# Kernel tuning notes

Hardware: AMD Instinct MI355X
Metric: run time of the kernel (lower is better)

Reference implementation:

```python
import jax, jax.numpy as jnp
import numpy as np

N = 50000
E = 800000
D = 128
L = 2


def setup_inputs() -> dict:
    key = jax.random.key(0)
    k0, k1, k2 = jax.random.split(key, 3)
    x = jax.random.normal(k0, (N, D), dtype=jnp.float32)
    edge_index = jax.random.randint(k1, (2, E), 0, N, dtype=jnp.int64)
    # GCNConv weights: one [D, D] matrix + bias per layer (dim_in -> dim_in)
    W = jax.random.normal(k2, (L, D, D), dtype=jnp.float32) * (1.0 / np.sqrt(D))
    b = jnp.zeros((L, D), dtype=jnp.float32)
    return {"x": x, "edge_index": edge_index, "W": W, "b": b}


def reference(x, edge_index, W, b):
    """Stacked GCNConv + relu (dropout is identity in eval mode).

    GCNConv: out = D^{-1/2} (A + I) D^{-1/2} (X W) + b, with self-loops added.
    """
    n = x.shape[0]
    loops = jnp.arange(n, dtype=edge_index.dtype)
    src = jnp.concatenate([edge_index[0], loops])  # [E + N]
    dst = jnp.concatenate([edge_index[1], loops])  # [E + N]
    # Degree (with self-loops) based symmetric normalization
    deg = jax.ops.segment_sum(jnp.ones_like(dst, dtype=x.dtype), dst, num_segments=n)
    dinv = jax.lax.rsqrt(deg)  # deg >= 1 thanks to self-loops
    coef = (dinv[src] * dinv[dst])[:, None]  # [E + N, 1]

    num_layers = W.shape[0]
    for i in range(num_layers):
        h = x @ W[i]  # transform first, as PyG GCNConv does
        x = jax.ops.segment_sum(h[src] * coef, dst, num_segments=n) + b[i]
        x = jax.nn.relu(x)
        # F.dropout with training=False is identity
    return x
```

## Files before the change

kernel.cpp:

```cpp
#include <hip/hip_runtime.h>
#include <hip/hip_fp16.h>


#define D 128
#define WP 136
#define YP 136
#define ABI 8
#define AGT 32
#define NB_SCAN 196

typedef _Float16 half8 __attribute__((ext_vector_type(8)));
typedef float floatx4 __attribute__((ext_vector_type(4)));


__global__ void count_kernel(const int* __restrict__ dst, int* deg8,
                             int* __restrict__ rank, int e, int n) {
    int i = blockIdx.x * blockDim.x + threadIdx.x;
    int c = (blockIdx.x & 7) * n;
    if (i < e) rank[i] = atomicAdd(&deg8[c + dst[i]], 1);
}

__global__ __launch_bounds__(256) void scanA_cvtw_kernel(const int* __restrict__ deg8,
                                                         int* __restrict__ degT,
                                                         int* __restrict__ base8,
                                                         int* __restrict__ partial,
                                                         int n, int nbs,
                                                         const float* __restrict__ W,
                                                         __half* __restrict__ WhT) {
    __shared__ int red[4];
    int tid = threadIdx.x;
    int bid = blockIdx.x;
    if (bid < nbs) {
        int i = bid * 256 + tid;
        int tot = 0;
        if (i < n) {
            int run = 0;
#pragma unroll
            for (int c = 0; c < 8; ++c) {
                base8[c * n + i] = run;
                run += deg8[c * n + i];
            }
            degT[i] = run;
            tot = run;
        }
        for (int off = 32; off > 0; off >>= 1) tot += __shfl_down(tot, off, 64);
        if ((tid & 63) == 0) red[tid >> 6] = tot;
        __syncthreads();
        if (tid == 0) partial[bid] = red[0] + red[1] + red[2] + red[3];
    } else {
        int id = (bid - nbs) * 256 + tid;
        int l = id >> 14;
        int rem = id & 16383;
        int f = rem >> 7;
        int k = rem & 127;
        WhT[id] = __float2half(W[l * 16384 + k * 128 + f]);
    }
}

__global__ __launch_bounds__(256) void scanC2_kernel(const int* __restrict__ degT,
                                                     const int* __restrict__ partial,
                                                     int* __restrict__ row_ptr,
                                                     float* __restrict__ dinv, int n) {
    __shared__ int sc[256];
    __shared__ int scb[256];
    int tid = threadIdx.x;
    int bid = blockIdx.x;
    int p = (tid < NB_SCAN) ? partial[tid] : 0;
    scb[tid] = p;
    __syncthreads();
    for (int off = 1; off < 256; off <<= 1) {
        int v = (tid >= off) ? scb[tid - off] : 0;
        __syncthreads();
        scb[tid] += v;
        __syncthreads();
    }
    int i = bid * 256 + tid;
    int c = (i < n) ? degT[i] : 0;
    sc[tid] = c;
    __syncthreads();
    for (int off = 1; off < 256; off <<= 1) {
        int v = (tid >= off) ? sc[tid - off] : 0;
        __syncthreads();
        sc[tid] += v;
        __syncthreads();
    }
    if (i < n) {
        int base = ((bid == 0) ? 0 : scb[bid - 1]) + sc[tid] - c;
        row_ptr[i] = base;
        dinv[i] = rsqrtf((float)(c + 1));
    }
    if (bid == 0 && tid == 0) row_ptr[n] = scb[NB_SCAN - 1];
}


__device__ inline void gemm_body(int bid, int tid,
                                 const float* __restrict__ Xf,
                                 const __half* __restrict__ WhT,
                                 __half* __restrict__ Hh, int n,
                                 _Float16* wlds) {
#pragma unroll
    for (int q = 0; q < 8; ++q) {
        int idx = tid + q * 256;
        int row = idx >> 4;
        int col8 = (idx & 15) * 8;
        const uint2* gsrc = (const uint2*)(WhT + row * 128 + col8);
        uint2 a = gsrc[0];
        uint2 b = gsrc[1];
        uint2* ldst = (uint2*)(wlds + row * WP + col8);
        ldst[0] = a;
        ldst[1] = b;
    }
    __syncthreads();

    const int wave = tid >> 6;
    const int lane = tid & 63;
    const int m = lane & 15;
    const int quad = lane >> 4;

    const int node = bid * 64 + wave * 16 + m;
    const int node_ld = node < n ? node : (n - 1);

    half8 bfr[4];
#pragma unroll
    for (int k = 0; k < 4; ++k) {
        const float4* p = (const float4*)(Xf + (size_t)node_ld * 128 + k * 32 + quad * 8);
        float4 lo = p[0];
        float4 hi = p[1];
        half8 h;
        h[0] = (_Float16)lo.x; h[1] = (_Float16)lo.y;
        h[2] = (_Float16)lo.z; h[3] = (_Float16)lo.w;
        h[4] = (_Float16)hi.x; h[5] = (_Float16)hi.y;
        h[6] = (_Float16)hi.z; h[7] = (_Float16)hi.w;
        bfr[k] = h;
    }

    floatx4 acc[8];
#pragma unroll
    for (int f = 0; f < 8; ++f) acc[f] = (floatx4){0.f, 0.f, 0.f, 0.f};

#pragma unroll
    for (int f = 0; f < 8; ++f) {
#pragma unroll
        for (int k = 0; k < 4; ++k) {
            half8 a = *(const half8*)(wlds + (f * 16 + m) * WP + k * 32 + quad * 8);
            acc[f] = __builtin_amdgcn_mfma_f32_16x16x32_f16(a, bfr[k], acc[f], 0, 0, 0);
        }
    }

    if (node < n) {
#pragma unroll
        for (int f = 0; f < 8; ++f) {
            __half2 p0 = __floats2half2_rn(acc[f][0], acc[f][1]);
            __half2 p1 = __floats2half2_rn(acc[f][2], acc[f][3]);
            uint2 pk;
            pk.x = *(unsigned int*)&p0;
            pk.y = *(unsigned int*)&p1;
            *(uint2*)(Hh + (size_t)node * 128 + f * 16 + quad * 4) = pk;
        }
    }
}

__device__ inline void fill_body(int i,
                                 const int* __restrict__ src,
                                 const int* __restrict__ dst,
                                 const int* __restrict__ rank,
                                 const int* __restrict__ row_ptr,
                                 const int* __restrict__ base8,
                                 const float* __restrict__ dinv,
                                 int2* __restrict__ recs, int e, int n) {
    if (i < e) {
        int d = dst[i];
        int s = src[i];
        int c = (i >> 8) & 7;
        int pos = row_ptr[d] + base8[c * n + d] + rank[i];
        int2 rec;
        rec.x = s;
        rec.y = __float_as_int(dinv[s] * dinv[d]);
        recs[pos] = rec;
    }
}


__global__ __launch_bounds__(256) void gemmfill_kernel(const float* __restrict__ Xf,
                                                       const __half* __restrict__ WhT,
                                                       __half* __restrict__ Hh, int n, int nbg,
                                                       const int* __restrict__ src,
                                                       const int* __restrict__ dst,
                                                       const int* __restrict__ rank,
                                                       const int* __restrict__ row_ptr,
                                                       const int* __restrict__ base8,
                                                       const float* __restrict__ dinv,
                                                       int2* __restrict__ recs, int e) {
    __shared__ _Float16 wlds[128 * WP];
    int bid = blockIdx.x;
    int tid = threadIdx.x;
    if (bid < nbg) {
        gemm_body(bid, tid, Xf, WhT, Hh, n, wlds);
    } else {
        fill_body((bid - nbg) * 256 + tid, src, dst, rank, row_ptr, base8, dinv, recs, e, n);
    }
}


__device__ inline void unpack8(uint4 u, float* f) {
    union { unsigned int x; __half2 h; } a, b, c, d;
    a.x = u.x; b.x = u.y; c.x = u.z; d.x = u.w;
    float2 f0 = __half22float2(a.h);
    float2 f1 = __half22float2(b.h);
    float2 f2 = __half22float2(c.h);
    float2 f3 = __half22float2(d.h);
    f[0] = f0.x; f[1] = f0.y; f[2] = f1.x; f[3] = f1.y;
    f[4] = f2.x; f[5] = f2.y; f[6] = f3.x; f[7] = f3.y;
}

__device__ inline void agg_row_q(int v, int fl,
                                 const uint4* __restrict__ H16,
                                 const int2* __restrict__ recs,
                                 const int* __restrict__ row_ptr,
                                 const float* __restrict__ dinv,
                                 float* acc) {
    {
        float di = dinv[v];
        float selfc = di * di;
        uint4 hv = H16[(size_t)v * 16 + fl];
        float f[8]; unpack8(hv, f);
#pragma unroll
        for (int t = 0; t < 8; ++t) acc[t] = f[t] * selfc;
    }

    int e0 = row_ptr[v];
    int e1 = row_ptr[v + 1];
    int e = e0;
    for (; e + ABI <= e1; e += ABI) {
        int2 r[ABI]; uint4 hu[ABI];
#pragma unroll
        for (int j = 0; j < ABI; ++j) r[j] = recs[e + j];
#pragma unroll
        for (int j = 0; j < ABI; ++j) hu[j] = H16[(size_t)r[j].x * 16 + fl];
#pragma unroll
        for (int j = 0; j < ABI; ++j) {
            float c = __int_as_float(r[j].y);
            float f[8]; unpack8(hu[j], f);
#pragma unroll
            for (int t = 0; t < 8; ++t) acc[t] = fmaf(f[t], c, acc[t]);
        }
    }
    if (e < e1) {
        int2 r[ABI]; uint4 hu[ABI]; bool act[ABI];
#pragma unroll
        for (int j = 0; j < ABI; ++j) {
            act[j] = (e + j) < e1;
            if (act[j]) r[j] = recs[e + j];
        }
#pragma unroll
        for (int j = 0; j < ABI; ++j) {
            if (act[j]) hu[j] = H16[(size_t)r[j].x * 16 + fl];
        }
#pragma unroll
        for (int j = 0; j < ABI; ++j) {
            if (act[j]) {
                float c = __int_as_float(r[j].y);
                float f[8]; unpack8(hu[j], f);
#pragma unroll
                for (int t = 0; t < 8; ++t) acc[t] = fmaf(f[t], c, acc[t]);
            }
        }
    }
}

__global__ __launch_bounds__(256, 4) void agg_kernel(const __half* __restrict__ H,
                                                     const int2* __restrict__ recs,
                                                     const int* __restrict__ row_ptr,
                                                     const float* __restrict__ dinv,
                                                     const float* __restrict__ bias,
                                                     float* __restrict__ YF, int n) {
    int wave = threadIdx.x >> 6;
    int lane = threadIdx.x & 63;
    int qw = lane >> 4;
    int fl = lane & 15;
    int v = blockIdx.x * 16 + wave * 4 + qw;
    if (v >= n) return;

    const uint4* H16 = (const uint4*)H;
    float acc[8];
    agg_row_q(v, fl, H16, recs, row_ptr, dinv, acc);

    const float4* B4 = (const float4*)bias;
    float4 b0 = B4[fl * 2];
    float4 b1 = B4[fl * 2 + 1];
    float4* Y4 = (float4*)YF;
    Y4[(size_t)v * 32 + fl * 2] = make_float4(
        fmaxf(acc[0] + b0.x, 0.f), fmaxf(acc[1] + b0.y, 0.f),
        fmaxf(acc[2] + b0.z, 0.f), fmaxf(acc[3] + b0.w, 0.f));
    Y4[(size_t)v * 32 + fl * 2 + 1] = make_float4(
        fmaxf(acc[4] + b1.x, 0.f), fmaxf(acc[5] + b1.y, 0.f),
        fmaxf(acc[6] + b1.z, 0.f), fmaxf(acc[7] + b1.w, 0.f));
}

__global__ __launch_bounds__(512, 4) void aggemm_kernel(
    const __half* __restrict__ H,
    const int2* __restrict__ recs,
    const int* __restrict__ row_ptr,
    const float* __restrict__ dinv,
    const float* __restrict__ bias,
    const __half* __restrict__ WhT2,
    __half* __restrict__ H2, int n) {
    __shared__ _Float16 yt[AGT * YP];
    const int tid = threadIdx.x;
    const int wave = tid >> 6;
    const int lane = tid & 63;
    const int qw = lane >> 4;
    const int fl = lane & 15;
    const int g = blockIdx.x;
    const uint4* H16 = (const uint4*)H;

    {
        const float4* B4 = (const float4*)bias;
        float4 b0 = B4[fl * 2];
        float4 b1 = B4[fl * 2 + 1];
        int r = wave * 4 + qw;
        int v = g * AGT + r;
        if (v < n) {
            float acc[8];
            agg_row_q(v, fl, H16, recs, row_ptr, dinv, acc);
            __half2 p0 = __floats2half2_rn(fmaxf(acc[0] + b0.x, 0.f), fmaxf(acc[1] + b0.y, 0.f));
            __half2 p1 = __floats2half2_rn(fmaxf(acc[2] + b0.z, 0.f), fmaxf(acc[3] + b0.w, 0.f));
            __half2 p2 = __floats2half2_rn(fmaxf(acc[4] + b1.x, 0.f), fmaxf(acc[5] + b1.y, 0.f));
            __half2 p3 = __floats2half2_rn(fmaxf(acc[6] + b1.z, 0.f), fmaxf(acc[7] + b1.w, 0.f));
            uint4 pk;
            pk.x = *(unsigned int*)&p0;
            pk.y = *(unsigned int*)&p1;
            pk.z = *(unsigned int*)&p2;
            pk.w = *(unsigned int*)&p3;
            *(uint4*)&yt[r * YP + fl * 8] = pk;
        } else {
            uint4 z = make_uint4(0, 0, 0, 0);
            *(uint4*)&yt[r * YP + fl * 8] = z;
        }
    }
    __syncthreads();

    const int mg = wave & 1;
    const int fh = wave >> 1;
    const int node = g * AGT + mg * 16 + fl;

    half8 bfr[4];
#pragma unroll
    for (int k = 0; k < 4; ++k)
        bfr[k] = *(const half8*)&yt[(mg * 16 + fl) * YP + k * 32 + qw * 8];

#pragma unroll
    for (int fb = 0; fb < 2; ++fb) {
        int f = fh * 2 + fb;
        floatx4 a4 = (floatx4){0.f, 0.f, 0.f, 0.f};
#pragma unroll
        for (int k = 0; k < 4; ++k) {
            half8 a = *(const half8*)(WhT2 + ((f * 16 + fl) * 128 + k * 32 + qw * 8));
            a4 = __builtin_amdgcn_mfma_f32_16x16x32_f16(a, bfr[k], a4, 0, 0, 0);
        }
        if (node < n) {
            __half2 p0 = __floats2half2_rn(a4[0], a4[1]);
            __half2 p1 = __floats2half2_rn(a4[2], a4[3]);
            uint2 pk;
            pk.x = *(unsigned int*)&p0;
            pk.y = *(unsigned int*)&p1;
            *(uint2*)(H2 + (size_t)node * 128 + f * 16 + qw * 4) = pk;
        }
    }
}


extern "C" void kernel_launch(void* const* d_in, const int* in_sizes, int n_in,
                              void* d_out, int out_size, void* d_ws, size_t ws_size,
                              hipStream_t stream) {
    const float* x = (const float*)d_in[0];
    const int* ei = (const int*)d_in[1];
    const float* W = (const float*)d_in[2];
    const float* b = (const float*)d_in[3];
    float* out = (float*)d_out;

    const int N = in_sizes[0] / D;
    const int E = in_sizes[1] / 2;

    const int* src = ei;
    const int* dst = ei + E;

    int* wsi = (int*)d_ws;
    float* wsf = (float*)d_ws;
    const size_t o_deg8 = 0;
    const size_t o_degT = o_deg8 + 400000;
    const size_t o_dinv = o_degT + 50000;
    const size_t o_rp   = o_dinv + 50000;
    const size_t o_part = o_rp + 50016;
    const size_t o_boff = o_part + 256;
    const size_t o_b8   = o_boff + 256;
    const size_t o_rank = o_b8 + 400000;
    const size_t o_rec  = o_rank + 800000;
    const size_t o_h    = o_rec + 1600000;
    const size_t o_wht  = o_h + 3200000;
    const size_t o_h2   = o_wht + 16384;

    int* deg8    = wsi + o_deg8;
    int* degT    = wsi + o_degT;
    float* dinv  = wsf + o_dinv;
    int* row_ptr = wsi + o_rp;
    int* partial = wsi + o_part;
    int* base8   = wsi + o_b8;
    int* rank    = wsi + o_rank;
    int2* recs   = (int2*)(wsi + o_rec);
    __half* h    = (__half*)(wsi + o_h);
    __half* wht  = (__half*)(wsi + o_wht);
    __half* h2   = (__half*)(wsi + o_h2);

    const int nb_e = (E + 255) / 256;
    const int nb_s = (N + 255) / 256;
    const int nb_g = (N + 63) / 64;
    const int nb_ag = (N + AGT - 1) / AGT;
    const int nb_a = (N + 15) / 16;

    hipMemsetAsync(deg8, 0, (size_t)8 * 50000 * sizeof(int), stream);
    count_kernel<<<nb_e, 256, 0, stream>>>(dst, deg8, rank, E, N);
    scanA_cvtw_kernel<<<nb_s + 128, 256, 0, stream>>>(deg8, degT, base8, partial,
                                                      N, nb_s, W, wht);
    scanC2_kernel<<<nb_s, 256, 0, stream>>>(degT, partial, row_ptr, dinv, N);
    gemmfill_kernel<<<nb_g + nb_e, 256, 0, stream>>>(x, wht, h, N, nb_g,
                                                     src, dst, rank, row_ptr, base8,
                                                     dinv, recs, E);
    aggemm_kernel<<<nb_ag, 512, 0, stream>>>(h, recs, row_ptr, dinv, b,
                                             wht + 16384, h2, N);
    agg_kernel<<<nb_a, 256, 0, stream>>>(h2, recs, row_ptr, dinv, b + D, out, N);
}
```

Measured before the change: 218.1 us.

## Split each node's edge list across two lane groups and combine via shuffle

Both aggregation kernels now assign two 16-lane groups to each destination node. Each group handles half of the node's edge range, and the partial sums are combined with a cross-lane xor shuffle. Rows per block drop from 32 to 16 in the fused agg+GEMM kernel, so each wave now computes one output feature tile instead of two. The aim is more parallelism and memory-level concurrency on the gather, which with about 16 edges per node is latency bound. The cost is twice as many threads and blocks, the added shuffles, and idle lanes in the final store.

```diff
diff --git a/kernel.cpp b/kernel.cpp
--- a/kernel.cpp
+++ b/kernel.cpp
@@ -6,7 +6,7 @@
 #define WP 136
 #define YP 136
 #define ABI 8
-#define AGT 32
+#define AGT 16
 #define NB_SCAN 196
 
 typedef _Float16 half8 __attribute__((ext_vector_type(8)));
@@ -213,25 +213,32 @@
     f[4] = f2.x; f[5] = f2.y; f[6] = f3.x; f[7] = f3.y;
 }
 
-__device__ inline void agg_row_q(int v, int fl,
-                                 const uint4* __restrict__ H16,
-                                 const int2* __restrict__ recs,
-                                 const int* __restrict__ row_ptr,
-                                 const float* __restrict__ dinv,
-                                 float* acc) {
-    {
+__device__ inline void agg_row_qh(int v, int fl, int half,
+                                  const uint4* __restrict__ H16,
+                                  const int2* __restrict__ recs,
+                                  const int* __restrict__ row_ptr,
+                                  const float* __restrict__ dinv,
+                                  float* acc) {
+    int e0 = row_ptr[v];
+    int e1 = row_ptr[v + 1];
+    int mid = e0 + ((e1 - e0 + 1) >> 1);
+    int eb = half ? mid : e0;
+    int ee = half ? e1 : mid;
+
+    if (half == 0) {
         float di = dinv[v];
         float selfc = di * di;
         uint4 hv = H16[(size_t)v * 16 + fl];
         float f[8]; unpack8(hv, f);
 #pragma unroll
         for (int t = 0; t < 8; ++t) acc[t] = f[t] * selfc;
-    }
-
-    int e0 = row_ptr[v];
-    int e1 = row_ptr[v + 1];
-    int e = e0;
-    for (; e + ABI <= e1; e += ABI) {
+    } else {
+#pragma unroll
+        for (int t = 0; t < 8; ++t) acc[t] = 0.f;
+    }
+
+    int e = eb;
+    for (; e + ABI <= ee; e += ABI) {
         int2 r[ABI]; uint4 hu[ABI];
 #pragma unroll
         for (int j = 0; j < ABI; ++j) r[j] = recs[e + j];
@@ -245,11 +252,11 @@
             for (int t = 0; t < 8; ++t) acc[t] = fmaf(f[t], c, acc[t]);
         }
     }
-    if (e < e1) {
+    if (e < ee) {
         int2 r[ABI]; uint4 hu[ABI]; bool act[ABI];
 #pragma unroll
         for (int j = 0; j < ABI; ++j) {
-            act[j] = (e + j) < e1;
+            act[j] = (e + j) < ee;
             if (act[j]) r[j] = recs[e + j];
         }
 #pragma unroll
@@ -278,23 +285,29 @@
     int lane = threadIdx.x & 63;
     int qw = lane >> 4;
     int fl = lane & 15;
-    int v = blockIdx.x * 16 + wave * 4 + qw;
+    int half = qw & 1;
+    int v = blockIdx.x * 8 + wave * 2 + (qw >> 1);
     if (v >= n) return;
 
     const uint4* H16 = (const uint4*)H;
     float acc[8];
-    agg_row_q(v, fl, H16, recs, row_ptr, dinv, acc);
-
-    const float4* B4 = (const float4*)bias;
-    float4 b0 = B4[fl * 2];
-    float4 b1 = B4[fl * 2 + 1];
-    float4* Y4 = (float4*)YF;
-    Y4[(size_t)v * 32 + fl * 2] = make_float4(
-        fmaxf(acc[0] + b0.x, 0.f), fmaxf(acc[1] + b0.y, 0.f),
-        fmaxf(acc[2] + b0.z, 0.f), fmaxf(acc[3] + b0.w, 0.f));
-    Y4[(size_t)v * 32 + fl * 2 + 1] = make_float4(
-        fmaxf(acc[4] + b1.x, 0.f), fmaxf(acc[5] + b1.y, 0.f),
-        fmaxf(acc[6] + b1.z, 0.f), fmaxf(acc[7] + b1.w, 0.f));
+    agg_row_qh(v, fl, half, H16, recs, row_ptr, dinv, acc);
+
+#pragma unroll
+    for (int t = 0; t < 8; ++t) acc[t] += __shfl_xor(acc[t], 16);
+
+    if (half == 0) {
+        const float4* B4 = (const float4*)bias;
+        float4 b0 = B4[fl * 2];
+        float4 b1 = B4[fl * 2 + 1];
+        float4* Y4 = (float4*)YF;
+        Y4[(size_t)v * 32 + fl * 2] = make_float4(
+            fmaxf(acc[0] + b0.x, 0.f), fmaxf(acc[1] + b0.y, 0.f),
+            fmaxf(acc[2] + b0.z, 0.f), fmaxf(acc[3] + b0.w, 0.f));
+        Y4[(size_t)v * 32 + fl * 2 + 1] = make_float4(
+            fmaxf(acc[4] + b1.x, 0.f), fmaxf(acc[5] + b1.y, 0.f),
+            fmaxf(acc[6] + b1.z, 0.f), fmaxf(acc[7] + b1.w, 0.f));
+    }
 }
 
 __global__ __launch_bounds__(512, 4) void aggemm_kernel(
@@ -311,61 +324,66 @@
     const int lane = tid & 63;
     const int qw = lane >> 4;
     const int fl = lane & 15;
+    const int half = qw & 1;
     const int g = blockIdx.x;
     const uint4* H16 = (const uint4*)H;
 
     {
-        const float4* B4 = (const float4*)bias;
-        float4 b0 = B4[fl * 2];
-        float4 b1 = B4[fl * 2 + 1];
-        int r = wave * 4 + qw;
+        int r = wave * 2 + (qw >> 1);
         int v = g * AGT + r;
+        float acc[8];
         if (v < n) {
-            float acc[8];
-            agg_row_q(v, fl, H16, recs, row_ptr, dinv, acc);
-            __half2 p0 = __floats2half2_rn(fmaxf(acc[0] + b0.x, 0.f), fmaxf(acc[1] + b0.y, 0.f));
-            __half2 p1 = __floats2half2_rn(fmaxf(acc[2] + b0.z, 0.f), fmaxf(acc[3] + b0.w, 0.f));
-            __half2 p2 = __floats2half2_rn(fmaxf(acc[4] + b1.x, 0.f), fmaxf(acc[5] + b1.y, 0.f));
-            __half2 p3 = __floats2half2_rn(fmaxf(acc[6] + b1.z, 0.f), fmaxf(acc[7] + b1.w, 0.f));
+            agg_row_qh(v, fl, half, H16, recs, row_ptr, dinv, acc);
+        } else {
+#pragma unroll
+            for (int t = 0; t < 8; ++t) acc[t] = 0.f;
+        }
+#pragma unroll
+        for (int t = 0; t < 8; ++t) acc[t] += __shfl_xor(acc[t], 16);
+
+        if (half == 0) {
             uint4 pk;
-            pk.x = *(unsigned int*)&p0;
-            pk.y = *(unsigned int*)&p1;
-            pk.z = *(unsigned int*)&p2;
-            pk.w = *(unsigned int*)&p3;
+            if (v < n) {
+                const float4* B4 = (const float4*)bias;
+                float4 b0 = B4[fl * 2];
+                float4 b1 = B4[fl * 2 + 1];
+                __half2 p0 = __floats2half2_rn(fmaxf(acc[0] + b0.x, 0.f), fmaxf(acc[1] + b0.y, 0.f));
+                __half2 p1 = __floats2half2_rn(fmaxf(acc[2] + b0.z, 0.f), fmaxf(acc[3] + b0.w, 0.f));
+                __half2 p2 = __floats2half2_rn(fmaxf(acc[4] + b1.x, 0.f), fmaxf(acc[5] + b1.y, 0.f));
+                __half2 p3 = __floats2half2_rn(fmaxf(acc[6] + b1.z, 0.f), fmaxf(acc[7] + b1.w, 0.f));
+                pk.x = *(unsigned int*)&p0;
+                pk.y = *(unsigned int*)&p1;
+                pk.z = *(unsigned int*)&p2;
+                pk.w = *(unsigned int*)&p3;
+            } else {
+                pk = make_uint4(0, 0, 0, 0);
+            }
             *(uint4*)&yt[r * YP + fl * 8] = pk;
-        } else {
-            uint4 z = make_uint4(0, 0, 0, 0);
-            *(uint4*)&yt[r * YP + fl * 8] = z;
         }
     }
     __syncthreads();
 
-    const int mg = wave & 1;
-    const int fh = wave >> 1;
-    const int node = g * AGT + mg * 16 + fl;
+    const int node = g * AGT + fl;
+    const int f = wave;
 
     half8 bfr[4];
 #pragma unroll
     for (int k = 0; k < 4; ++k)
-        bfr[k] = *(const half8*)&yt[(mg * 16 + fl) * YP + k * 32 + qw * 8];
-
-#pragma unroll
-    for (int fb = 0; fb < 2; ++fb) {
-        int f = fh * 2 + fb;
-        floatx4 a4 = (floatx4){0.f, 0.f, 0.f, 0.f};
-#pragma unroll
-        for (int k = 0; k < 4; ++k) {
-            half8 a = *(const half8*)(WhT2 + ((f * 16 + fl) * 128 + k * 32 + qw * 8));
-            a4 = __builtin_amdgcn_mfma_f32_16x16x32_f16(a, bfr[k], a4, 0, 0, 0);
-        }
-        if (node < n) {
-            __half2 p0 = __floats2half2_rn(a4[0], a4[1]);
-            __half2 p1 = __floats2half2_rn(a4[2], a4[3]);
-            uint2 pk;
-            pk.x = *(unsigned int*)&p0;
-            pk.y = *(unsigned int*)&p1;
-            *(uint2*)(H2 + (size_t)node * 128 + f * 16 + qw * 4) = pk;
-        }
+        bfr[k] = *(const half8*)&yt[fl * YP + k * 32 + qw * 8];
+
+    floatx4 a4 = (floatx4){0.f, 0.f, 0.f, 0.f};
+#pragma unroll
+    for (int k = 0; k < 4; ++k) {
+        half8 a = *(const half8*)(WhT2 + ((f * 16 + fl) * 128 + k * 32 + qw * 8));
+        a4 = __builtin_amdgcn_mfma_f32_16x16x32_f16(a, bfr[k], a4, 0, 0, 0);
+    }
+    if (node < n) {
+        __half2 p0 = __floats2half2_rn(a4[0], a4[1]);
+        __half2 p1 = __floats2half2_rn(a4[2], a4[3]);
+        uint2 pk;
+        pk.x = *(unsigned int*)&p0;
+        pk.y = *(unsigned int*)&p1;
+        *(uint2*)(H2 + (size_t)node * 128 + f * 16 + qw * 4) = pk;
     }
 }
 
@@ -416,7 +434,7 @@
     const int nb_s = (N + 255) / 256;
     const int nb_g = (N + 63) / 64;
     const int nb_ag = (N + AGT - 1) / AGT;
-    const int nb_a = (N + 15) / 16;
+    const int nb_a = (N + 7) / 8;
 
     hipMemsetAsync(deg8, 0, (size_t)8 * 50000 * sizeof(int), stream);
     count_kernel<<<nb_e, 256, 0, stream>>>(dst, deg8, rank, E, N);
```

After: 224.3 us. 2.8% more time.
